# Performance work log

Measured on AMD Instinct MI355X. Metric: run time of the kernel, lower is better.

## Reference

```python
import jax, jax.numpy as jnp
import numpy as np

B, T_OBS, H, L, D = 4096, 8, 512, 2, 2


def _gates(x, h, c, Wih, Whh, b):
    # PyTorch LSTM gate order: i, f, g, o
    g = x @ Wih.T + h @ Whh.T + b
    i, f, gg, o = jnp.split(g, 4, axis=-1)
    c_new = jax.nn.sigmoid(f) * c + jax.nn.sigmoid(i) * jnp.tanh(gg)
    h_new = jax.nn.sigmoid(o) * jnp.tanh(c_new)
    return h_new, c_new


def _run_lstm(x, Wih, Whh, b):
    # stacked batch_first LSTM, zero initial state; x: [B,T,H]
    n_layers = Wih.shape[0]
    hs, cs = [], []
    for l in range(n_layers):
        def step(carry, xt, l=l):
            h, c = carry
            h, c = _gates(xt, h, c, Wih[l], Whh[l], b[l])
            return (h, c), h
        init = (jnp.zeros((x.shape[0], Whh.shape[-1]), x.dtype),
                jnp.zeros((x.shape[0], Whh.shape[-1]), x.dtype))
        (h, c), ys = jax.lax.scan(step, init, jnp.swapaxes(x, 0, 1))
        x = jnp.swapaxes(ys, 0, 1)
        hs.append(h)
        cs.append(c)
    return x, jnp.stack(hs), jnp.stack(cs)


def setup_inputs() -> dict:
    key = jax.random.key(0)
    ks = jax.random.split(key, 12)
    s = 1.0 / np.sqrt(H)
    inp = {
        "obs": jax.random.normal(ks[0], (B, T_OBS, D), jnp.float32),
        "obsVel": jax.random.normal(ks[1], (B, T_OBS, D), jnp.float32),
        "mean": jax.random.normal(ks[2], (D,), jnp.float32),
        "std": jnp.ones((D,), jnp.float32),
        "pred_len": 12,
        "enc_W": jax.random.normal(ks[3], (D, H), jnp.float32) * s,
        "enc_b": jnp.zeros((H,), jnp.float32),
        "dec_W": jax.random.normal(ks[4], (H, D), jnp.float32) * s,
        "dec_b": jnp.zeros((D,), jnp.float32),
        "lstm_Wih": jax.random.normal(ks[5], (L, 4 * H, H), jnp.float32) * s,
        "lstm_Whh": jax.random.normal(ks[6], (L, 4 * H, H), jnp.float32) * s,
        "lstm_b": jnp.zeros((L, 4 * H), jnp.float32),
        "cell_Wih": jax.random.normal(ks[7], (L, 4 * H, H), jnp.float32) * s,
        "cell_Whh": jax.random.normal(ks[8], (L, 4 * H, H), jnp.float32) * s,
        "cell_b": jnp.zeros((L, 4 * H), jnp.float32),
    }
    return inp


def reference(obs, obsVel, mean, std, pred_len, enc_W, enc_b, dec_W, dec_b,
              lstm_Wih, lstm_Whh, lstm_b, cell_Wih, cell_Whh, cell_b):
    inp = (obsVel - mean) / std                      # [B,T,2]
    embed = inp @ enc_W + enc_b                      # [B,T,H]
    output, hs, cs = _run_lstm(embed, lstm_Wih, lstm_Whh, lstm_b)
    inner = output[:, -1, :]                         # [B,H]

    def decode_step(carry, _):
        hs, cs, inner = carry
        def layer(inner, xs):
            Wih, Whh, b, h, c = xs
            h2, c2 = _gates(inner, h, c, Wih, Whh, b)
            return h2, (h2, c2)
        inner2, (hs2, cs2) = jax.lax.scan(
            layer, inner, (cell_Wih, cell_Whh, cell_b, hs, cs))
        return (hs2, cs2, inner2), inner2

    _, steps = jax.lax.scan(decode_step, (hs, cs, inner), None,
                            length=pred_len - 1)     # [P-1,B,H]
    predlist = jnp.concatenate([output[:, -1:, :], jnp.swapaxes(steps, 0, 1)],
                               axis=1)               # [B,P,H]
    outVelocity = predlist @ dec_W + dec_b           # [B,P,2]
    pred = outVelocity[:, :, :2] * std + mean
    pred = jnp.cumsum(pred, axis=1) + obs[:, -1:, :]
    return pred
```

## Files before the change

kernel.cpp:

```cpp
#include <hip/hip_runtime.h>
#include <hip/hip_bf16.h>

typedef __attribute__((ext_vector_type(8))) short bf16x8;
typedef __attribute__((ext_vector_type(4))) float f32x4;

#define MFMA16(a,b,c) __builtin_amdgcn_mfma_f32_16x16x32_bf16(a,b,c,0,0,0)

__device__ inline ushort f2bf(float f){
  union { float f; uint u; } v; v.f = f;
  uint r = v.u + 0x7FFFu + ((v.u >> 16) & 1u);
  return (ushort)(r >> 16);
}
__device__ inline float sigf(float x){ return 1.f/(1.f+__expf(-x)); }
__device__ inline float tanhf_(float x){ return 2.f/(1.f+__expf(-2.f*x)) - 1.f; }

__device__ inline void gload_lds16(const ushort* g, ushort* lds){
  __builtin_amdgcn_global_load_lds(
      (const __attribute__((address_space(1))) void*)g,
      (__attribute__((address_space(3))) void*)lds, 16, 0, 0);
}

__global__ void convert_weights(const float* __restrict__ s0, const float* __restrict__ s1,
                                const float* __restrict__ s2, const float* __restrict__ s3,
                                ushort* __restrict__ dst){
  size_t i4 = ((size_t)blockIdx.x*256 + threadIdx.x)*4;
  int tsel = (int)(i4 >> 21);
  const float* s = (tsel & 2) ? ((tsel & 1) ? s3 : s2) : ((tsel & 1) ? s1 : s0);
  size_t off = i4 & 2097151u;
  float4 v = *(const float4*)&s[off];
  ushort4 o; o.x=f2bf(v.x); o.y=f2bf(v.y); o.z=f2bf(v.z); o.w=f2bf(v.w);
  *(ushort4*)&dst[i4] = o;
}

__global__ void embed_kernel(const float* __restrict__ obsVel, const float* __restrict__ mean,
                             const float* __restrict__ stdv, const float* __restrict__ encW,
                             const float* __restrict__ encb, ushort* __restrict__ embed){
  int idx = blockIdx.x*256 + threadIdx.x;
  int row = idx >> 6, c8 = (idx & 63) * 8;
  float x0 = (obsVel[row*2+0] - mean[0]) / stdv[0];
  float x1 = (obsVel[row*2+1] - mean[1]) / stdv[1];
  ushort o[8];
  #pragma unroll
  for (int j=0;j<8;j++){
    int col = c8 + j;
    o[j] = f2bf(x0*encW[col] + x1*encW[512+col] + encb[col]);
  }
  *(uint4*)&embed[(size_t)row*512 + c8] = *(const uint4*)o;
}

#define NKT_SEG 8

__global__ __launch_bounds__(256, 2) void lstm_cell_kernel(
    const ushort* __restrict__ A0, int lda0,
    const ushort* __restrict__ A1, int lda1,
    const ushort* __restrict__ B0,
    const ushort* __restrict__ B1,
    const float*  __restrict__ bias,
    float* __restrict__ C,
    ushort* __restrict__ H0, int ldh0,
    ushort* __restrict__ H1, int ldh1,
    int nSeg, int czero)
{
  __shared__ ushort bL[2][8192];
  const int tid = threadIdx.x;
  const int w = tid >> 6, lane = tid & 63;
  const int bm = blockIdx.y * 128;
  const int bn = blockIdx.x * 32;

  f32x4 acc[2][8];
  #pragma unroll
  for (int m=0;m<2;m++)
    #pragma unroll
    for (int n=0;n<8;n++) acc[m][n] = (f32x4)0.f;

  int boff[4], ldsO[4];
  #pragma unroll
  for (int p=0;p<4;p++){
    int i = p*256 + tid;
    int r = i>>3, s = i&7, ch = s ^ (r&7);
    boff[p] = (((r>>5)<<9) + bn + (r&31))*512 + ch*8;
    ldsO[p] = (p*256 + (tid & ~63)) * 8;
  }

  const int arow0 = bm + w*32 + (lane&15);
  const int arow1 = arow0 + 16;
  const int ca = (lane>>4)*8;

  int bOff[8];
  #pragma unroll
  for (int n=0;n<8;n++){
    int row = (n>>1)*32 + (n&1)*16 + (lane&15);
    int slot = (lane>>4) ^ (row&7);
    bOff[n] = row*64 + slot*8;
  }

  #define STAGE_B(bi, kt) do { \
    const ushort* Bseg = ((kt) < NKT_SEG) ? B0 : B1; \
    const int k0_ = ((kt) & (NKT_SEG-1)) << 6; \
    _Pragma("unroll") \
    for (int p=0;p<4;p++) \
      gload_lds16(Bseg + boff[p] + k0_, &bL[bi][ldsO[p]]); \
  } while(0)

  #define LOAD_A(AF, kt) do { \
    const ushort* Aseg = ((kt) < NKT_SEG) ? A0 : A1; \
    const int lda_     = ((kt) < NKT_SEG) ? lda0 : lda1; \
    const int k0_ = ((kt) & (NKT_SEG-1)) << 6; \
    const ushort* pa0_ = Aseg + (size_t)arow0*lda_ + k0_ + ca; \
    const ushort* pa1_ = Aseg + (size_t)arow1*lda_ + k0_ + ca; \
    AF[0][0] = *(const bf16x8*)pa0_;  AF[0][1] = *(const bf16x8*)(pa0_+32); \
    AF[1][0] = *(const bf16x8*)pa1_;  AF[1][1] = *(const bf16x8*)(pa1_+32); \
  } while(0)

  #define COMPUTE(bi, AF) do { \
    bf16x8 bfr[8]; \
    _Pragma("unroll") \
    for (int n=0;n<8;n++) bfr[n] = *(const bf16x8*)&bL[bi][bOff[n]]; \
    __builtin_amdgcn_s_setprio(1); \
    _Pragma("unroll") \
    for (int m=0;m<2;m++) \
      _Pragma("unroll") \
      for (int n=0;n<8;n++) acc[m][n] = MFMA16(AF[m][0], bfr[n], acc[m][n]); \
    __builtin_amdgcn_s_setprio(0); \
    _Pragma("unroll") \
    for (int n=0;n<8;n++) bfr[n] = *(const bf16x8*)&bL[bi][bOff[n]^32]; \
    __builtin_amdgcn_s_setprio(1); \
    _Pragma("unroll") \
    for (int m=0;m<2;m++) \
      _Pragma("unroll") \
      for (int n=0;n<8;n++) acc[m][n] = MFMA16(AF[m][1], bfr[n], acc[m][n]); \
    __builtin_amdgcn_s_setprio(0); \
  } while(0)

  const int nkt = nSeg * NKT_SEG;
  bf16x8 afA[2][2], afB[2][2];

  STAGE_B(0, 0);
  LOAD_A(afA, 0);
  __syncthreads();

  for (int kt = 0; kt < nkt-2; kt += 2){
    STAGE_B(1, kt+1);  LOAD_A(afB, kt+1);
    COMPUTE(0, afA);
    __syncthreads();
    STAGE_B(0, kt+2);  LOAD_A(afA, kt+2);
    COMPUTE(1, afB);
    __syncthreads();
  }
  STAGE_B(1, nkt-1);  LOAD_A(afB, nkt-1);
  COMPUTE(0, afA);
  __syncthreads();
  COMPUTE(1, afB);

  #undef STAGE_B
  #undef LOAD_A
  #undef COMPUTE

  const int r0 = bm + w*32 + ((lane>>4)<<2);
  #pragma unroll
  for (int cc=0;cc<2;cc++){
    const int ccol = bn + cc*16 + (lane&15);
    const float bi = bias[ccol];
    const float bff = bias[512+ccol];
    const float bg = bias[1024+ccol];
    const float bo = bias[1536+ccol];
    #pragma unroll
    for (int m=0;m<2;m++){
      #pragma unroll
      for (int reg=0;reg<4;reg++){
        const int row = r0 + m*16 + reg;
        float gi = acc[m][0+cc][reg] + bi;
        float gf = acc[m][2+cc][reg] + bff;
        float gg = acc[m][4+cc][reg] + bg;
        float go = acc[m][6+cc][reg] + bo;
        size_t cidx = (size_t)row*512 + ccol;
        float cv = czero ? 0.f : C[cidx];
        float cn = sigf(gf)*cv + sigf(gi)*tanhf_(gg);
        float hv = sigf(go)*tanhf_(cn);
        C[cidx] = cn;
        ushort hb = f2bf(hv);
        H0[(size_t)row*ldh0 + ccol] = hb;
        if (H1) H1[(size_t)row*ldh1 + ccol] = hb;
      }
    }
  }
}

__global__ void final_kernel(const ushort* __restrict__ pred, const float* __restrict__ decW,
                             const float* __restrict__ decb, const float* __restrict__ mean,
                             const float* __restrict__ stdv, const float* __restrict__ obs,
                             float* __restrict__ out){
  int w = threadIdx.x >> 6, lane = threadIdx.x & 63;
  int b = blockIdx.x*4 + w;
  float w0[8], w1[8];
  #pragma unroll
  for (int j=0;j<8;j++){
    int k = lane*8 + j;
    w0[j] = decW[k*2+0];
    w1[j] = decW[k*2+1];
  }
  float cum0 = 0.f, cum1 = 0.f;
  float m0 = mean[0], m1 = mean[1], sv0 = stdv[0], sv1 = stdv[1];
  float o0 = obs[(b*8+7)*2+0], o1 = obs[(b*8+7)*2+1];
  float db0 = decb[0], db1 = decb[1];
  for (int t=0;t<12;t++){
    const uint4 q = *(const uint4*)&pred[((size_t)b*12+t)*512 + lane*8];
    uint u[4] = {q.x,q.y,q.z,q.w};
    float s0=0.f, s1=0.f;
    #pragma unroll
    for (int p=0;p<4;p++){
      float lo = __uint_as_float(u[p]<<16);
      float hi = __uint_as_float(u[p]&0xffff0000u);
      s0 += lo*w0[2*p] + hi*w0[2*p+1];
      s1 += lo*w1[2*p] + hi*w1[2*p+1];
    }
    #pragma unroll
    for (int off=32; off>0; off>>=1){ s0 += __shfl_down(s0, off); s1 += __shfl_down(s1, off); }
    if (lane==0){
      cum0 += (s0+db0)*sv0 + m0;
      cum1 += (s1+db1)*sv1 + m1;
      out[((size_t)b*12+t)*2+0] = cum0 + o0;
      out[((size_t)b*12+t)*2+1] = cum1 + o1;
    }
  }
}

extern "C" void kernel_launch(void* const* d_in, const int* in_sizes, int n_in,
                              void* d_out, int out_size, void* d_ws, size_t ws_size,
                              hipStream_t stream) {
  const float* obs      = (const float*)d_in[0];
  const float* obsVel   = (const float*)d_in[1];
  const float* mean     = (const float*)d_in[2];
  const float* stdv     = (const float*)d_in[3];
  const float* encW     = (const float*)d_in[5];
  const float* encb     = (const float*)d_in[6];
  const float* decW     = (const float*)d_in[7];
  const float* decb     = (const float*)d_in[8];
  const float* lstm_Wih = (const float*)d_in[9];
  const float* lstm_Whh = (const float*)d_in[10];
  const float* lstm_b   = (const float*)d_in[11];
  const float* cell_Wih = (const float*)d_in[12];
  const float* cell_Whh = (const float*)d_in[13];
  const float* cell_b   = (const float*)d_in[14];

  char* ws = (char*)d_ws;
  ushort* wbf   = (ushort*)ws;
  ushort* embed = (ushort*)(ws + (16ull<<20));
  ushort* h0[2] = {(ushort*)(ws + (48ull<<20)), (ushort*)(ws + (52ull<<20))};
  ushort* h1[2] = {(ushort*)(ws + (56ull<<20)), (ushort*)(ws + (60ull<<20))};
  float*  c0    = (float*)(ws + (64ull<<20));
  float*  c1    = (float*)(ws + (72ull<<20));
  ushort* pred  = (ushort*)(ws + (80ull<<20));

  ushort* w_lstm_ih = wbf;
  ushort* w_lstm_hh = wbf + 2097152;
  ushort* w_cell_ih = wbf + 4194304;
  ushort* w_cell_hh = wbf + 6291456;

  convert_weights<<<8192, 256, 0, stream>>>(lstm_Wih, lstm_Whh, cell_Wih, cell_Whh, wbf);
  embed_kernel<<<8192, 256, 0, stream>>>(obsVel, mean, stdv, encW, encb, embed);

  dim3 grid(16, 32);
  int cur0 = 0, cur1 = 0;
  for (int t=0;t<8;t++){
    int ns = (t==0) ? 1 : 2;
    int cz = (t==0) ? 1 : 0;
    lstm_cell_kernel<<<grid, 256, 0, stream>>>(embed + t*512, 4096, h0[cur0], 512,
        w_lstm_ih, w_lstm_hh, lstm_b, c0, h0[cur0^1], 512, (ushort*)nullptr, 0, ns, cz);
    lstm_cell_kernel<<<grid, 256, 0, stream>>>(h0[cur0^1], 512, h1[cur1], 512,
        w_lstm_ih + 1048576, w_lstm_hh + 1048576, lstm_b + 2048, c1, h1[cur1^1], 512,
        (t==7) ? pred : (ushort*)nullptr, 6144, ns, cz);
    cur0 ^= 1; cur1 ^= 1;
  }
  for (int s=1;s<12;s++){
    lstm_cell_kernel<<<grid, 256, 0, stream>>>(pred + (s-1)*512, 6144, h0[cur0], 512,
        w_cell_ih, w_cell_hh, cell_b, c0, h0[cur0^1], 512, (ushort*)nullptr, 0, 2, 0);
    lstm_cell_kernel<<<grid, 256, 0, stream>>>(h0[cur0^1], 512, h1[cur1], 512,
        w_cell_ih + 1048576, w_cell_hh + 1048576, cell_b + 2048, c1, h1[cur1^1], 512,
        pred + s*512, 6144, 2, 0);
    cur0 ^= 1; cur1 ^= 1;
  }
  final_kernel<<<1024, 256, 0, stream>>>(pred, decW, decb, mean, stdv, obs, (float*)d_out);
}
```

Before: 1.122 ms.

## Load B fragments directly from global into registers, dropping LDS staging

The LSTM cell GEMM kernel no longer stages weight tiles through shared memory with async global-to-LDS loads and barriers. Each wave now reads its A and B fragments straight from global memory into registers, double-buffered in registers across a fully unrolled k-loop per segment. This removes the LDS round trip and the __syncthreads calls. In exchange, the four waves in a block now each fetch the same B data separately, leaning on L1/L2 for reuse, and register pressure rises.

```diff
diff --git a/kernel.cpp b/kernel.cpp
--- a/kernel.cpp
+++ b/kernel.cpp
@@ -13,12 +13,6 @@
 }
 __device__ inline float sigf(float x){ return 1.f/(1.f+__expf(-x)); }
 __device__ inline float tanhf_(float x){ return 2.f/(1.f+__expf(-2.f*x)) - 1.f; }
-
-__device__ inline void gload_lds16(const ushort* g, ushort* lds){
-  __builtin_amdgcn_global_load_lds(
-      (const __attribute__((address_space(1))) void*)g,
-      (__attribute__((address_space(3))) void*)lds, 16, 0, 0);
-}
 
 __global__ void convert_weights(const float* __restrict__ s0, const float* __restrict__ s1,
                                 const float* __restrict__ s2, const float* __restrict__ s3,
@@ -48,7 +42,7 @@
   *(uint4*)&embed[(size_t)row*512 + c8] = *(const uint4*)o;
 }
 
-#define NKT_SEG 8
+#define KSTEPS 16
 
 __global__ __launch_bounds__(256, 2) void lstm_cell_kernel(
     const ushort* __restrict__ A0, int lda0,
@@ -61,7 +55,6 @@
     ushort* __restrict__ H1, int ldh1,
     int nSeg, int czero)
 {
-  __shared__ ushort bL[2][8192];
   const int tid = threadIdx.x;
   const int w = tid >> 6, lane = tid & 63;
   const int bm = blockIdx.y * 128;
@@ -73,88 +66,53 @@
     #pragma unroll
     for (int n=0;n<8;n++) acc[m][n] = (f32x4)0.f;
 
-  int boff[4], ldsO[4];
-  #pragma unroll
-  for (int p=0;p<4;p++){
-    int i = p*256 + tid;
-    int r = i>>3, s = i&7, ch = s ^ (r&7);
-    boff[p] = (((r>>5)<<9) + bn + (r&31))*512 + ch*8;
-    ldsO[p] = (p*256 + (tid & ~63)) * 8;
-  }
-
+  const int kq = (lane >> 4) * 8;
   const int arow0 = bm + w*32 + (lane&15);
   const int arow1 = arow0 + 16;
-  const int ca = (lane>>4)*8;
-
-  int bOff[8];
+  size_t boff[8];
   #pragma unroll
   for (int n=0;n<8;n++){
-    int row = (n>>1)*32 + (n&1)*16 + (lane&15);
-    int slot = (lane>>4) ^ (row&7);
-    bOff[n] = row*64 + slot*8;
-  }
-
-  #define STAGE_B(bi, kt) do { \
-    const ushort* Bseg = ((kt) < NKT_SEG) ? B0 : B1; \
-    const int k0_ = ((kt) & (NKT_SEG-1)) << 6; \
+    int grow = (n>>1)*512 + bn + (n&1)*16 + (lane&15);
+    boff[n] = (size_t)grow*512 + kq;
+  }
+
+  #define LOADF(AF, BF, Aseg, lda_, Bseg, kt) do { \
+    const int k0_ = (kt) << 5; \
+    AF[0] = *(const bf16x8*)(Aseg + (size_t)arow0*lda_ + k0_ + kq); \
+    AF[1] = *(const bf16x8*)(Aseg + (size_t)arow1*lda_ + k0_ + kq); \
     _Pragma("unroll") \
-    for (int p=0;p<4;p++) \
-      gload_lds16(Bseg + boff[p] + k0_, &bL[bi][ldsO[p]]); \
+    for (int n=0;n<8;n++) BF[n] = *(const bf16x8*)(Bseg + boff[n] + k0_); \
   } while(0)
 
-  #define LOAD_A(AF, kt) do { \
-    const ushort* Aseg = ((kt) < NKT_SEG) ? A0 : A1; \
-    const int lda_     = ((kt) < NKT_SEG) ? lda0 : lda1; \
-    const int k0_ = ((kt) & (NKT_SEG-1)) << 6; \
-    const ushort* pa0_ = Aseg + (size_t)arow0*lda_ + k0_ + ca; \
-    const ushort* pa1_ = Aseg + (size_t)arow1*lda_ + k0_ + ca; \
-    AF[0][0] = *(const bf16x8*)pa0_;  AF[0][1] = *(const bf16x8*)(pa0_+32); \
-    AF[1][0] = *(const bf16x8*)pa1_;  AF[1][1] = *(const bf16x8*)(pa1_+32); \
-  } while(0)
-
-  #define COMPUTE(bi, AF) do { \
-    bf16x8 bfr[8]; \
-    _Pragma("unroll") \
-    for (int n=0;n<8;n++) bfr[n] = *(const bf16x8*)&bL[bi][bOff[n]]; \
+  #define MFMA_ALL(AF, BF) do { \
     __builtin_amdgcn_s_setprio(1); \
     _Pragma("unroll") \
     for (int m=0;m<2;m++) \
       _Pragma("unroll") \
-      for (int n=0;n<8;n++) acc[m][n] = MFMA16(AF[m][0], bfr[n], acc[m][n]); \
-    __builtin_amdgcn_s_setprio(0); \
-    _Pragma("unroll") \
-    for (int n=0;n<8;n++) bfr[n] = *(const bf16x8*)&bL[bi][bOff[n]^32]; \
-    __builtin_amdgcn_s_setprio(1); \
-    _Pragma("unroll") \
-    for (int m=0;m<2;m++) \
-      _Pragma("unroll") \
-      for (int n=0;n<8;n++) acc[m][n] = MFMA16(AF[m][1], bfr[n], acc[m][n]); \
+      for (int n=0;n<8;n++) acc[m][n] = MFMA16(AF[m], BF[n], acc[m][n]); \
     __builtin_amdgcn_s_setprio(0); \
   } while(0)
 
-  const int nkt = nSeg * NKT_SEG;
-  bf16x8 afA[2][2], afB[2][2];
-
-  STAGE_B(0, 0);
-  LOAD_A(afA, 0);
-  __syncthreads();
-
-  for (int kt = 0; kt < nkt-2; kt += 2){
-    STAGE_B(1, kt+1);  LOAD_A(afB, kt+1);
-    COMPUTE(0, afA);
-    __syncthreads();
-    STAGE_B(0, kt+2);  LOAD_A(afA, kt+2);
-    COMPUTE(1, afB);
-    __syncthreads();
-  }
-  STAGE_B(1, nkt-1);  LOAD_A(afB, nkt-1);
-  COMPUTE(0, afA);
-  __syncthreads();
-  COMPUTE(1, afB);
-
-  #undef STAGE_B
-  #undef LOAD_A
-  #undef COMPUTE
+  bf16x8 aA[2], bA[8], aB[2], bB[8];
+
+  for (int seg=0; seg<nSeg; ++seg){
+    const ushort* Aseg = seg ? A1 : A0;
+    const int lda_     = seg ? lda1 : lda0;
+    const ushort* Bseg = seg ? B1 : B0;
+    LOADF(aA, bA, Aseg, lda_, Bseg, 0);
+    #pragma unroll
+    for (int kt=0; kt<KSTEPS-2; kt+=2){
+      LOADF(aB, bB, Aseg, lda_, Bseg, kt+1);
+      MFMA_ALL(aA, bA);
+      LOADF(aA, bA, Aseg, lda_, Bseg, kt+2);
+      MFMA_ALL(aB, bB);
+    }
+    LOADF(aB, bB, Aseg, lda_, Bseg, KSTEPS-1);
+    MFMA_ALL(aA, bA);
+    MFMA_ALL(aB, bB);
+  }
+  #undef LOADF
+  #undef MFMA_ALL
 
   const int r0 = bm + w*32 + ((lane>>4)<<2);
   #pragma unroll
```

New measurement: 2.970 ms. 2.65x slower.

## Switch LSTM cell GEMM to 32x32x16 MFMA with 2x2 warp tiling

Applied to the files above, without the earlier changes.

Replaces the 16x16x32 bf16 MFMA tiling, where each wave covered 32 rows and all four gates, with 32x32x16 MFMA on a 2x2 wave grid. Each wave now computes a 64x64 tile, so fewer LDS reads of B fragments and fewer MFMA instructions are needed per k-step. Because each wave no longer holds all four gates for its rows, accumulators are exchanged through LDS after the main loop so each wave gets i,f,g,o for its 32 rows. This adds an epilogue shuffle and a barrier, and raises A-fragment register use.

```diff
diff --git a/kernel.cpp b/kernel.cpp
--- a/kernel.cpp
+++ b/kernel.cpp
@@ -3,8 +3,9 @@
 
 typedef __attribute__((ext_vector_type(8))) short bf16x8;
 typedef __attribute__((ext_vector_type(4))) float f32x4;
-
-#define MFMA16(a,b,c) __builtin_amdgcn_mfma_f32_16x16x32_bf16(a,b,c,0,0,0)
+typedef __attribute__((ext_vector_type(16))) float f32x16;
+
+#define MFMA32(a,b,c) __builtin_amdgcn_mfma_f32_32x32x16_bf16(a,b,c,0,0,0)
 
 __device__ inline ushort f2bf(float f){
   union { float f; uint u; } v; v.f = f;
@@ -64,125 +65,146 @@
   __shared__ ushort bL[2][8192];
   const int tid = threadIdx.x;
   const int w = tid >> 6, lane = tid & 63;
+  const int wr = w >> 1, wc = w & 1;
   const int bm = blockIdx.y * 128;
   const int bn = blockIdx.x * 32;
 
-  f32x4 acc[2][8];
+  f32x16 acc[2][2];
   #pragma unroll
   for (int m=0;m<2;m++)
     #pragma unroll
-    for (int n=0;n<8;n++) acc[m][n] = (f32x4)0.f;
-
-  int boff[4], ldsO[4];
+    for (int n=0;n<2;n++) acc[m][n] = (f32x16)0.f;
+
+  size_t bsrc[4]; int ldsO[4];
   #pragma unroll
   for (int p=0;p<4;p++){
     int i = p*256 + tid;
-    int r = i>>3, s = i&7, ch = s ^ (r&7);
-    boff[p] = (((r>>5)<<9) + bn + (r&31))*512 + ch*8;
+    int r = i>>3, s = i&7, c = s ^ (r&7);
+    bsrc[p] = (size_t)((r>>5)*512 + bn + (r&31))*512 + c*8;
     ldsO[p] = (p*256 + (tid & ~63)) * 8;
   }
 
-  const int arow0 = bm + w*32 + (lane&15);
-  const int arow1 = arow0 + 16;
-  const int ca = (lane>>4)*8;
-
-  int bOff[8];
-  #pragma unroll
-  for (int n=0;n<8;n++){
-    int row = (n>>1)*32 + (n&1)*16 + (lane&15);
-    int slot = (lane>>4) ^ (row&7);
-    bOff[n] = row*64 + slot*8;
-  }
+  int bOff[2][4];
+  #pragma unroll
+  for (int nf=0;nf<2;nf++){
+    int r = (2*wc+nf)*32 + (lane&31);
+    #pragma unroll
+    for (int ks=0;ks<4;ks++){
+      int slot = (ks*2 + (lane>>5)) ^ (r&7);
+      bOff[nf][ks] = r*64 + slot*8;
+    }
+  }
+
+  const int ar0 = bm + wr*64 + (lane&31);
+  const int ar1 = ar0 + 32;
+  const int ak  = (lane>>5)*8;
 
   #define STAGE_B(bi, kt) do { \
     const ushort* Bseg = ((kt) < NKT_SEG) ? B0 : B1; \
     const int k0_ = ((kt) & (NKT_SEG-1)) << 6; \
     _Pragma("unroll") \
     for (int p=0;p<4;p++) \
-      gload_lds16(Bseg + boff[p] + k0_, &bL[bi][ldsO[p]]); \
+      gload_lds16(Bseg + bsrc[p] + k0_, &bL[bi][ldsO[p]]); \
   } while(0)
 
   #define LOAD_A(AF, kt) do { \
     const ushort* Aseg = ((kt) < NKT_SEG) ? A0 : A1; \
     const int lda_     = ((kt) < NKT_SEG) ? lda0 : lda1; \
-    const int k0_ = ((kt) & (NKT_SEG-1)) << 6; \
-    const ushort* pa0_ = Aseg + (size_t)arow0*lda_ + k0_ + ca; \
-    const ushort* pa1_ = Aseg + (size_t)arow1*lda_ + k0_ + ca; \
-    AF[0][0] = *(const bf16x8*)pa0_;  AF[0][1] = *(const bf16x8*)(pa0_+32); \
-    AF[1][0] = *(const bf16x8*)pa1_;  AF[1][1] = *(const bf16x8*)(pa1_+32); \
+    const int k0_ = (((kt) & (NKT_SEG-1)) << 6) + ak; \
+    const ushort* p0_ = Aseg + (size_t)ar0*lda_ + k0_; \
+    const ushort* p1_ = Aseg + (size_t)ar1*lda_ + k0_; \
+    _Pragma("unroll") \
+    for (int ks=0;ks<4;ks++){ \
+      AF[0][ks] = *(const bf16x8*)(p0_ + ks*16); \
+      AF[1][ks] = *(const bf16x8*)(p1_ + ks*16); \
+    } \
   } while(0)
 
   #define COMPUTE(bi, AF) do { \
-    bf16x8 bfr[8]; \
-    _Pragma("unroll") \
-    for (int n=0;n<8;n++) bfr[n] = *(const bf16x8*)&bL[bi][bOff[n]]; \
-    __builtin_amdgcn_s_setprio(1); \
-    _Pragma("unroll") \
-    for (int m=0;m<2;m++) \
-      _Pragma("unroll") \
-      for (int n=0;n<8;n++) acc[m][n] = MFMA16(AF[m][0], bfr[n], acc[m][n]); \
-    __builtin_amdgcn_s_setprio(0); \
-    _Pragma("unroll") \
-    for (int n=0;n<8;n++) bfr[n] = *(const bf16x8*)&bL[bi][bOff[n]^32]; \
-    __builtin_amdgcn_s_setprio(1); \
-    _Pragma("unroll") \
-    for (int m=0;m<2;m++) \
-      _Pragma("unroll") \
-      for (int n=0;n<8;n++) acc[m][n] = MFMA16(AF[m][1], bfr[n], acc[m][n]); \
-    __builtin_amdgcn_s_setprio(0); \
+    _Pragma("unroll") \
+    for (int ks=0;ks<4;ks++){ \
+      bf16x8 b0_ = *(const bf16x8*)&bL[bi][bOff[0][ks]]; \
+      bf16x8 b1_ = *(const bf16x8*)&bL[bi][bOff[1][ks]]; \
+      __builtin_amdgcn_s_setprio(1); \
+      acc[0][0] = MFMA32(AF[0][ks], b0_, acc[0][0]); \
+      acc[0][1] = MFMA32(AF[0][ks], b1_, acc[0][1]); \
+      acc[1][0] = MFMA32(AF[1][ks], b0_, acc[1][0]); \
+      acc[1][1] = MFMA32(AF[1][ks], b1_, acc[1][1]); \
+      __builtin_amdgcn_s_setprio(0); \
+    } \
   } while(0)
 
   const int nkt = nSeg * NKT_SEG;
-  bf16x8 afA[2][2], afB[2][2];
+  bf16x8 aA[2][4], aB[2][4];
 
   STAGE_B(0, 0);
-  LOAD_A(afA, 0);
+  LOAD_A(aA, 0);
   __syncthreads();
 
-  for (int kt = 0; kt < nkt-2; kt += 2){
-    STAGE_B(1, kt+1);  LOAD_A(afB, kt+1);
-    COMPUTE(0, afA);
+  for (int kt=0; kt<nkt; kt+=2){
+    STAGE_B(1, kt+1);  LOAD_A(aB, kt+1);
+    COMPUTE(0, aA);
     __syncthreads();
-    STAGE_B(0, kt+2);  LOAD_A(afA, kt+2);
-    COMPUTE(1, afB);
+    if (kt+2 < nkt){ STAGE_B(0, kt+2); LOAD_A(aA, kt+2); }
+    COMPUTE(1, aB);
     __syncthreads();
   }
-  STAGE_B(1, nkt-1);  LOAD_A(afB, nkt-1);
-  COMPUTE(0, afA);
-  __syncthreads();
-  COMPUTE(1, afB);
-
   #undef STAGE_B
   #undef LOAD_A
   #undef COMPUTE
 
-  const int r0 = bm + w*32 + ((lane>>4)<<2);
-  #pragma unroll
-  for (int cc=0;cc<2;cc++){
-    const int ccol = bn + cc*16 + (lane&15);
-    const float bi = bias[ccol];
-    const float bff = bias[512+ccol];
-    const float bg = bias[1024+ccol];
-    const float bo = bias[1536+ccol];
-    #pragma unroll
-    for (int m=0;m<2;m++){
-      #pragma unroll
-      for (int reg=0;reg<4;reg++){
-        const int row = r0 + m*16 + reg;
-        float gi = acc[m][0+cc][reg] + bi;
-        float gf = acc[m][2+cc][reg] + bff;
-        float gg = acc[m][4+cc][reg] + bg;
-        float go = acc[m][6+cc][reg] + bo;
-        size_t cidx = (size_t)row*512 + ccol;
-        float cv = czero ? 0.f : C[cidx];
-        float cn = sigf(gf)*cv + sigf(gi)*tanhf_(gg);
-        float hv = sigf(go)*tanhf_(cn);
-        C[cidx] = cn;
-        ushort hb = f2bf(hv);
-        H0[(size_t)row*ldh0 + ccol] = hb;
-        if (H1) H1[(size_t)row*ldh1 + ccol] = hb;
-      }
-    }
+  float* xch = (float*)bL;
+  #define XWRITE(V, PW, PM, PN) do { \
+    float* pl_ = xch + (((((PW)*2+(PM))*2)+(PN))<<10); \
+    _Pragma("unroll") \
+    for (int q=0;q<4;q++){ \
+      f32x4 v_; v_[0]=(V)[q*4]; v_[1]=(V)[q*4+1]; v_[2]=(V)[q*4+2]; v_[3]=(V)[q*4+3]; \
+      *(f32x4*)(pl_ + q*256 + lane*4) = v_; \
+    } \
+  } while(0)
+  #define XREAD(V, PW, PM, PN) do { \
+    float* pl_ = xch + (((((PW)*2+(PM))*2)+(PN))<<10); \
+    _Pragma("unroll") \
+    for (int q=0;q<4;q++){ \
+      f32x4 v_ = *(f32x4*)(pl_ + q*256 + lane*4); \
+      (V)[q*4]=v_[0]; (V)[q*4+1]=v_[1]; (V)[q*4+2]=v_[2]; (V)[q*4+3]=v_[3]; \
+    } \
+  } while(0)
+
+  if (wc == 0){ XWRITE(acc[1][0], wr, 1, 0); XWRITE(acc[1][1], wr, 1, 1); }
+  else        { XWRITE(acc[0][0], wr, 0, 0); XWRITE(acc[0][1], wr, 0, 1); }
+  __syncthreads();
+  f32x16 fA, fB;
+  XREAD(fA, wr, wc, 0);
+  XREAD(fB, wr, wc, 1);
+  #undef XWRITE
+  #undef XREAD
+
+  f32x16 gI, gF, gG, gO;
+  if (wc == 0){ gI = acc[0][0]; gF = acc[0][1]; gG = fA; gO = fB; }
+  else        { gI = fA;        gF = fB;        gG = acc[1][0]; gO = acc[1][1]; }
+
+  const int colc = bn + (lane&31);
+  const float b_i = bias[colc];
+  const float b_f = bias[512+colc];
+  const float b_g = bias[1024+colc];
+  const float b_o = bias[1536+colc];
+  const int rbase = bm + wr*64 + wc*32 + ((lane>>5)<<2);
+  #pragma unroll
+  for (int reg=0;reg<16;reg++){
+    const int row = rbase + (reg&3) + ((reg>>2)<<3);
+    float gi = gI[reg] + b_i;
+    float gf = gF[reg] + b_f;
+    float gg = gG[reg] + b_g;
+    float go = gO[reg] + b_o;
+    size_t cidx = (size_t)row*512 + colc;
+    float cv = czero ? 0.f : C[cidx];
+    float cn = sigf(gf)*cv + sigf(gi)*tanhf_(gg);
+    float hv = sigf(go)*tanhf_(cn);
+    C[cidx] = cn;
+    ushort hb = f2bf(hv);
+    H0[(size_t)row*ldh0 + colc] = hb;
+    if (H1) H1[(size_t)row*ldh1 + colc] = hb;
   }
 }
 
```

Result: slower. 1.796 ms (+60.1%).

## Triple-buffer LSTM GEMM B tiles with counted waits and prefetch cell state

Applied to the files above, without the earlier changes.

The weight-tile staging in LDS goes from double to triple buffering, with B staged two k-steps ahead. Full __syncthreads are replaced by explicit s_waitcnt vmcnt plus s_barrier, so one load group can stay in flight across the barrier. Bias and the previous cell state C are loaded into registers before the GEMM loop, which keeps their latency out of the epilogue. The cost is 48KB of LDS per block instead of 32KB, more registers, and waits that depend on hand-counted vmcnt values.

```diff
diff --git a/kernel.cpp b/kernel.cpp
--- a/kernel.cpp
+++ b/kernel.cpp
@@ -61,11 +61,40 @@
     ushort* __restrict__ H1, int ldh1,
     int nSeg, int czero)
 {
-  __shared__ ushort bL[2][8192];
+  __shared__ ushort bL[3][8192];
   const int tid = threadIdx.x;
   const int w = tid >> 6, lane = tid & 63;
   const int bm = blockIdx.y * 128;
   const int bn = blockIdx.x * 32;
+
+  const int r0 = bm + w*32 + ((lane>>4)<<2);
+  float br[2][4], creg[2][2][4];
+  #pragma unroll
+  for (int cc=0;cc<2;cc++){
+    const int ccol = bn + cc*16 + (lane&15);
+    br[cc][0] = bias[ccol];
+    br[cc][1] = bias[512+ccol];
+    br[cc][2] = bias[1024+ccol];
+    br[cc][3] = bias[1536+ccol];
+  }
+  if (czero){
+    #pragma unroll
+    for (int cc=0;cc<2;cc++)
+      #pragma unroll
+      for (int m=0;m<2;m++)
+        #pragma unroll
+        for (int reg=0;reg<4;reg++) creg[cc][m][reg] = 0.f;
+  } else {
+    #pragma unroll
+    for (int cc=0;cc<2;cc++){
+      const int ccol = bn + cc*16 + (lane&15);
+      #pragma unroll
+      for (int m=0;m<2;m++)
+        #pragma unroll
+        for (int reg=0;reg<4;reg++)
+          creg[cc][m][reg] = C[(size_t)(r0 + m*16 + reg)*512 + ccol];
+    }
+  }
 
   f32x4 acc[2][8];
   #pragma unroll
@@ -105,9 +134,9 @@
   #define LOAD_A(AF, kt) do { \
     const ushort* Aseg = ((kt) < NKT_SEG) ? A0 : A1; \
     const int lda_     = ((kt) < NKT_SEG) ? lda0 : lda1; \
-    const int k0_ = ((kt) & (NKT_SEG-1)) << 6; \
-    const ushort* pa0_ = Aseg + (size_t)arow0*lda_ + k0_ + ca; \
-    const ushort* pa1_ = Aseg + (size_t)arow1*lda_ + k0_ + ca; \
+    const int k0_ = (((kt) & (NKT_SEG-1)) << 6) + ca; \
+    const ushort* pa0_ = Aseg + (size_t)arow0*lda_ + k0_; \
+    const ushort* pa1_ = Aseg + (size_t)arow1*lda_ + k0_; \
     AF[0][0] = *(const bf16x8*)pa0_;  AF[0][1] = *(const bf16x8*)(pa0_+32); \
     AF[1][0] = *(const bf16x8*)pa1_;  AF[1][1] = *(const bf16x8*)(pa1_+32); \
   } while(0)
@@ -132,38 +161,48 @@
     __builtin_amdgcn_s_setprio(0); \
   } while(0)
 
+  #define SYNC_CNT(N) do { \
+    __builtin_amdgcn_sched_barrier(0); \
+    asm volatile("s_waitcnt vmcnt(" #N ")" ::: "memory"); \
+    __builtin_amdgcn_s_barrier(); \
+    __builtin_amdgcn_sched_barrier(0); \
+  } while(0)
+
   const int nkt = nSeg * NKT_SEG;
-  bf16x8 afA[2][2], afB[2][2];
+  bf16x8 aA[2][2], aB[2][2];
+  int b0 = 0, b1 = 1, b2 = 2;
 
   STAGE_B(0, 0);
-  LOAD_A(afA, 0);
-  __syncthreads();
+  STAGE_B(1, 1);
+  LOAD_A(aA, 0);
+  SYNC_CNT(8);
 
   for (int kt = 0; kt < nkt-2; kt += 2){
-    STAGE_B(1, kt+1);  LOAD_A(afB, kt+1);
-    COMPUTE(0, afA);
-    __syncthreads();
-    STAGE_B(0, kt+2);  LOAD_A(afA, kt+2);
-    COMPUTE(1, afB);
-    __syncthreads();
-  }
-  STAGE_B(1, nkt-1);  LOAD_A(afB, nkt-1);
-  COMPUTE(0, afA);
-  __syncthreads();
-  COMPUTE(1, afB);
+    STAGE_B(b2, kt+2);
+    LOAD_A(aB, kt+1);
+    COMPUTE(b0, aA);
+    SYNC_CNT(8);
+    { int t_ = b0; b0 = b1; b1 = b2; b2 = t_; }
+    STAGE_B(b2, kt+3 < nkt ? kt+3 : kt+2);
+    LOAD_A(aA, kt+2);
+    COMPUTE(b0, aB);
+    SYNC_CNT(8);
+    { int t_ = b0; b0 = b1; b1 = b2; b2 = t_; }
+  }
+  LOAD_A(aB, nkt-1);
+  COMPUTE(b0, aA);
+  SYNC_CNT(4);
+  COMPUTE(b1, aB);
 
   #undef STAGE_B
   #undef LOAD_A
   #undef COMPUTE
-
-  const int r0 = bm + w*32 + ((lane>>4)<<2);
+  #undef SYNC_CNT
+
   #pragma unroll
   for (int cc=0;cc<2;cc++){
     const int ccol = bn + cc*16 + (lane&15);
-    const float bi = bias[ccol];
-    const float bff = bias[512+ccol];
-    const float bg = bias[1024+ccol];
-    const float bo = bias[1536+ccol];
+    const float bi = br[cc][0], bff = br[cc][1], bg = br[cc][2], bo = br[cc][3];
     #pragma unroll
     for (int m=0;m<2;m++){
       #pragma unroll
@@ -173,11 +212,9 @@
         float gf = acc[m][2+cc][reg] + bff;
         float gg = acc[m][4+cc][reg] + bg;
         float go = acc[m][6+cc][reg] + bo;
-        size_t cidx = (size_t)row*512 + ccol;
-        float cv = czero ? 0.f : C[cidx];
-        float cn = sigf(gf)*cv + sigf(gi)*tanhf_(gg);
+        float cn = sigf(gf)*creg[cc][m][reg] + sigf(gi)*tanhf_(gg);
         float hv = sigf(go)*tanhf_(cn);
-        C[cidx] = cn;
+        C[(size_t)row*512 + ccol] = cn;
         ushort hb = f2bf(hv);
         H0[(size_t)row*ldh0 + ccol] = hb;
         if (H1) H1[(size_t)row*ldh1 + ccol] = hb;
```

Result: no change. 1.111 ms (-1.0%).
